# Optimization experiments

Measured on AMD Instinct MI355X. Metric: run time of the kernel, lower is better.

## Reference

```python
import jax, jax.numpy as jnp
import numpy as np

N, D = 8192, 256

def _gram_rbf(x, y, sigma):
    x2 = jnp.sum(x * x, axis=-1)                      # [N]
    y2 = jnp.sum(y * y, axis=-1)                      # [M]
    xy = jnp.einsum('nd,md->nm', x, y)                # [N,M] GEMM
    sq = x2[:, None] + y2[None, :] - 2.0 * xy
    return jnp.exp(-sq / sigma)

def setup_inputs() -> dict:
    key = jax.random.key(0)
    k1, k2 = jax.random.split(key)
    return {
        'input': jax.random.normal(k1, (N, D), dtype=jnp.float32),
        'target': jax.random.normal(k2, (N, D), dtype=jnp.float32) + 0.5,
        'sigma': 256,
    }

def reference(input, target, sigma):
    XX = _gram_rbf(input, input, sigma)
    YY = _gram_rbf(target, target, sigma)
    XY = _gram_rbf(input, target, sigma)
    return jnp.mean(XX) + jnp.mean(YY) - 2.0 * jnp.mean(XY)
```

## Files before the change

kernel.cpp:

```cpp
#include <hip/hip_runtime.h>
#include <hip/hip_bf16.h>
#include <stdint.h>
#include <stddef.h>


#define N_PTS   8192
#define DIM     256
#define TWO_N   16384
#define CSTRIDE 20

#define AS1 __attribute__((address_space(1)))
#define AS3 __attribute__((address_space(3)))

typedef __attribute__((ext_vector_type(4))) float f32x4;
typedef __attribute__((ext_vector_type(4))) int   i32x4;
typedef __attribute__((ext_vector_type(8))) int   i32x8;

__global__ __launch_bounds__(256) void mmd_prep(const float* __restrict__ X,
                                                const float* __restrict__ Y,
                                                const int* __restrict__ sigmap,
                                                unsigned char* __restrict__ Zf8,
                                                float* __restrict__ n2,
                                                float* __restrict__ part) {
    if (blockIdx.x == 0 && threadIdx.x < 64) part[threadIdx.x] = 0.0f;

    const int wave = threadIdx.x >> 6;
    const int lane = threadIdx.x & 63;
    const int row  = blockIdx.x * 4 + wave;

    const float* src = (row < N_PTS) ? (X + (size_t)row * DIM)
                                     : (Y + (size_t)(row - N_PTS) * DIM);
    float4 v = ((const float4*)src)[lane];

    float s = v.x * v.x + v.y * v.y + v.z * v.z + v.w * v.w;
#pragma unroll
    for (int off = 32; off; off >>= 1) s += __shfl_down(s, off, 64);
    if (lane == 0) {
        const float c2 = -1.4426950408889634f / (float)(*sigmap);
        n2[row] = c2 * s;
    }

    const int p01 = __builtin_amdgcn_cvt_pk_fp8_f32(v.x, v.y, 0, false);
    const int p23 = __builtin_amdgcn_cvt_pk_fp8_f32(v.z, v.w, 0, false);
    const unsigned int pk = ((unsigned)p01 & 0xffffu) | ((unsigned)p23 << 16);
    *(unsigned int*)(Zf8 + (size_t)row * DIM + (size_t)lane * 4) = pk;
}

__global__ __launch_bounds__(256, 5) void mmd_main(const unsigned char* __restrict__ Zf8,
                                                   const float* __restrict__ n2,
                                                   const int* __restrict__ sigmap,
                                                   float* __restrict__ part) {
    __shared__ char smem_b[32768];

    const int bid = (int)blockIdx.x;
    const int p   = bid / CSTRIDE;
    const int cc  = bid % CSTRIDE;
    const int r0  = p;
    const int r1  = 127 - p;

    const int nT0 = (cc <= r0) ? ((r0 - cc) / CSTRIDE + 1) : 0;
    const int nT1 = (r1 - cc) / CSTRIDE + 1;
    const int nS0 = nT0 * 2;
    const int nS  = nS0 + nT1 * 2;

    const int t    = threadIdx.x;
    const int wave = t >> 6;
    const int lane = t & 63;
    const int g    = lane >> 4;
    const int ml   = lane & 15;

    const float m2 = 2.8853900817779268f / (float)(*sigmap);
    const int   SC = 0x7f7f7f7f;

    const int gbase = (t >> 4) * 256 + (((t & 15) ^ (t >> 4)) * 16);
    const int lbase = t * 16;

    int rb0[2], rb1[2];
#pragma unroll
    for (int kc = 0; kc < 2; ++kc) {
        rb0[kc] = ml * 256 + (((kc * 8 + g * 2)     ^ ml) * 16);
        rb1[kc] = ml * 256 + (((kc * 8 + g * 2 + 1) ^ ml) * 16);
    }

    i32x8 af[2][2];
    float a_i[2][4];
    auto loadA = [&](int rowTile) {
        const int rowBase = rowTile * 128;
#pragma unroll
        for (int mt = 0; mt < 2; ++mt) {
            const unsigned char* rp =
                Zf8 + (size_t)(rowBase + wave * 32 + mt * 16 + ml) * 256 + g * 32;
#pragma unroll
            for (int kc = 0; kc < 2; ++kc) {
                union { i32x4 h[2]; i32x8 v; } u;
                u.h[0] = *(const i32x4*)(rp + kc * 128);
                u.h[1] = *(const i32x4*)(rp + kc * 128 + 16);
                af[mt][kc] = u.v;
            }
        }
#pragma unroll
        for (int mt = 0; mt < 2; ++mt)
#pragma unroll
            for (int rr = 0; rr < 4; ++rr)
                a_i[mt][rr] = n2[rowBase + wave * 32 + mt * 16 + g * 4 + rr];
    };

    const int firstRow = nT0 ? r0 : r1;
    loadA(firstRow);
    int curRow = firstRow;

    const f32x4 zacc = {0.0f, 0.0f, 0.0f, 0.0f};

    auto sliceCol = [&](int s, int& rowT, int& bc, int& h) {
        int si;
        if (s < nS0) { rowT = r0; si = s; }
        else         { rowT = r1; si = s - nS0; }
        bc = cc + (si >> 1) * CSTRIDE;
        h  = si & 1;
    };

    {
        int rT, bc, h; sliceCol(0, rT, bc, h);
        const unsigned char* sb = Zf8 + (size_t)(bc * 128 + h * 64) * 256 + gbase;
#pragma unroll
        for (int i = 0; i < 4; ++i)
            __builtin_amdgcn_global_load_lds((const AS1 void*)(sb + i * 4096),
                                             (AS3 void*)(smem_b + i * 4096 + lbase), 16, 0, 0);
    }

    float block_acc = 0.0f;
    int cur = 0;

    for (int s = 0; s < nS; ++s) {
        int rowT, bc, h;
        sliceCol(s, rowT, bc, h);
        if (rowT != curRow) { loadA(rowT); curRow = rowT; }
        const int colBase = bc * 128 + h * 64;

        float eb[4];
#pragma unroll
        for (int nt = 0; nt < 4; ++nt)
            eb[nt] = __builtin_amdgcn_exp2f(n2[colBase + nt * 16 + ml]);

        __syncthreads();

        if (s + 1 < nS) {
            int rTN, bcN, hN;
            sliceCol(s + 1, rTN, bcN, hN);
            const unsigned char* sb =
                Zf8 + (size_t)(bcN * 128 + hN * 64) * 256 + gbase;
            char* dst = smem_b + (cur ^ 1) * 16384;
#pragma unroll
            for (int i = 0; i < 4; ++i)
                __builtin_amdgcn_global_load_lds((const AS1 void*)(sb + i * 4096),
                                                 (AS3 void*)(dst + i * 4096 + lbase), 16, 0, 0);
        }

        const char* buf = smem_b + cur * 16384;
        f32x4 acc[2][4];
#pragma unroll
        for (int nt = 0; nt < 4; ++nt) {
#pragma unroll
            for (int kc = 0; kc < 2; ++kc) {
                union { i32x4 hh[2]; i32x8 v; } u;
                u.hh[0] = *(const i32x4*)(buf + nt * 4096 + rb0[kc]);
                u.hh[1] = *(const i32x4*)(buf + nt * 4096 + rb1[kc]);
                const i32x8 bf = u.v;
#pragma unroll
                for (int mt = 0; mt < 2; ++mt)
                    acc[mt][nt] = __builtin_amdgcn_mfma_scale_f32_16x16x128_f8f6f4(
                        af[mt][kc], bf, (kc == 0) ? zacc : acc[mt][nt],
                        0, 0, 0, SC, 0, SC);
            }
        }

        float ts0 = 0.0f, ts1 = 0.0f, ts2 = 0.0f, ts3 = 0.0f;
#pragma unroll
        for (int mt = 0; mt < 2; ++mt)
#pragma unroll
            for (int nt = 0; nt < 4; ++nt) {
                const float e = eb[nt];
                ts0 = fmaf(__builtin_amdgcn_exp2f(fmaf(acc[mt][nt][0], m2, a_i[mt][0])), e, ts0);
                ts1 = fmaf(__builtin_amdgcn_exp2f(fmaf(acc[mt][nt][1], m2, a_i[mt][1])), e, ts1);
                ts2 = fmaf(__builtin_amdgcn_exp2f(fmaf(acc[mt][nt][2], m2, a_i[mt][2])), e, ts2);
                ts3 = fmaf(__builtin_amdgcn_exp2f(fmaf(acc[mt][nt][3], m2, a_i[mt][3])), e, ts3);
            }
        const float tsum = (ts0 + ts1) + (ts2 + ts3);

        const float sgn = ((bc < 64) == (rowT < 64)) ? 1.0f : -1.0f;
        const float w   = (bc == rowT) ? sgn : 2.0f * sgn;
        block_acc = fmaf(w, tsum, block_acc);
        cur ^= 1;
    }

    float s = block_acc;
#pragma unroll
    for (int off = 32; off; off >>= 1) s += __shfl_down(s, off, 64);
    if (lane == 0)
        atomicAdd(part + (bid & 63), s);
}

__global__ __launch_bounds__(64) void mmd_finish(const float* __restrict__ part,
                                                 float* __restrict__ out) {
    const int lane = threadIdx.x & 63;
    float s = part[lane];
#pragma unroll
    for (int off = 32; off; off >>= 1) s += __shfl_down(s, off, 64);
    if (lane == 0) out[0] = s * (1.0f / 67108864.0f);
}

extern "C" void kernel_launch(void* const* d_in, const int* in_sizes, int n_in,
                              void* d_out, int out_size, void* d_ws, size_t ws_size,
                              hipStream_t stream) {
    const float* X      = (const float*)d_in[0];
    const float* Y      = (const float*)d_in[1];
    const int*   sigmap = (const int*)d_in[2];
    float*       out    = (float*)d_out;

    unsigned char* Zf8  = (unsigned char*)d_ws;
    float*         n2   = (float*)((char*)d_ws + (size_t)TWO_N * DIM);
    float*         part = n2 + TWO_N;

    mmd_prep<<<TWO_N / 4, 256, 0, stream>>>(X, Y, sigmap, Zf8, n2, part);
    mmd_main<<<64 * CSTRIDE, 256, 0, stream>>>(Zf8, n2, sigmap, part);
    mmd_finish<<<1, 64, 0, stream>>>(part, out);
}
```

Baseline: 136.5 us.

## Load B tiles directly from global into registers and split work across 2048 blocks

Drops the double-buffered LDS staging of the B operand via global_load_lds and its per-slice barrier. Each wave now reads its B fragments straight from global memory (through L2/L1) into registers. The grid changes from 20 column strides to 16, and each block's slice list is split in two halves, giving 2048 blocks with occupancy hint 4. This removes the barrier and LDS traffic. The cost is that B is no longer shared across the four waves, so global and L1 loads are duplicated and load latency is exposed without explicit prefetch.

```diff
diff --git a/kernel.cpp b/kernel.cpp
--- a/kernel.cpp
+++ b/kernel.cpp
@@ -7,10 +7,6 @@
 #define N_PTS   8192
 #define DIM     256
 #define TWO_N   16384
-#define CSTRIDE 20
-
-#define AS1 __attribute__((address_space(1)))
-#define AS3 __attribute__((address_space(3)))
 
 typedef __attribute__((ext_vector_type(4))) float f32x4;
 typedef __attribute__((ext_vector_type(4))) int   i32x4;
@@ -46,22 +42,23 @@
     *(unsigned int*)(Zf8 + (size_t)row * DIM + (size_t)lane * 4) = pk;
 }
 
-__global__ __launch_bounds__(256, 5) void mmd_main(const unsigned char* __restrict__ Zf8,
+__global__ __launch_bounds__(256, 4) void mmd_main(const unsigned char* __restrict__ Zf8,
                                                    const float* __restrict__ n2,
                                                    const int* __restrict__ sigmap,
                                                    float* __restrict__ part) {
-    __shared__ char smem_b[32768];
-
     const int bid = (int)blockIdx.x;
-    const int p   = bid / CSTRIDE;
-    const int cc  = bid % CSTRIDE;
+    const int p   = bid >> 5;
+    const int cc  = (bid >> 1) & 15;
+    const int hb  = bid & 1;
     const int r0  = p;
     const int r1  = 127 - p;
 
-    const int nT0 = (cc <= r0) ? ((r0 - cc) / CSTRIDE + 1) : 0;
-    const int nT1 = (r1 - cc) / CSTRIDE + 1;
+    const int nT0 = (cc <= r0) ? (((r0 - cc) >> 4) + 1) : 0;
+    const int nT1 = ((r1 - cc) >> 4) + 1;
     const int nS0 = nT0 * 2;
     const int nS  = nS0 + nT1 * 2;
+    const int sBeg = hb ? (nS >> 1) : 0;
+    const int sEnd = hb ? nS : (nS >> 1);
 
     const int t    = threadIdx.x;
     const int wave = t >> 6;
@@ -71,16 +68,6 @@
 
     const float m2 = 2.8853900817779268f / (float)(*sigmap);
     const int   SC = 0x7f7f7f7f;
-
-    const int gbase = (t >> 4) * 256 + (((t & 15) ^ (t >> 4)) * 16);
-    const int lbase = t * 16;
-
-    int rb0[2], rb1[2];
-#pragma unroll
-    for (int kc = 0; kc < 2; ++kc) {
-        rb0[kc] = ml * 256 + (((kc * 8 + g * 2)     ^ ml) * 16);
-        rb1[kc] = ml * 256 + (((kc * 8 + g * 2 + 1) ^ ml) * 16);
-    }
 
     i32x8 af[2][2];
     float a_i[2][4];
@@ -105,33 +92,25 @@
                 a_i[mt][rr] = n2[rowBase + wave * 32 + mt * 16 + g * 4 + rr];
     };
 
-    const int firstRow = nT0 ? r0 : r1;
-    loadA(firstRow);
-    int curRow = firstRow;
-
-    const f32x4 zacc = {0.0f, 0.0f, 0.0f, 0.0f};
-
     auto sliceCol = [&](int s, int& rowT, int& bc, int& h) {
         int si;
         if (s < nS0) { rowT = r0; si = s; }
         else         { rowT = r1; si = s - nS0; }
-        bc = cc + (si >> 1) * CSTRIDE;
+        bc = cc + (si >> 1) * 16;
         h  = si & 1;
     };
 
-    {
-        int rT, bc, h; sliceCol(0, rT, bc, h);
-        const unsigned char* sb = Zf8 + (size_t)(bc * 128 + h * 64) * 256 + gbase;
-#pragma unroll
-        for (int i = 0; i < 4; ++i)
-            __builtin_amdgcn_global_load_lds((const AS1 void*)(sb + i * 4096),
-                                             (AS3 void*)(smem_b + i * 4096 + lbase), 16, 0, 0);
-    }
+    int rT0, bc0, h0;
+    sliceCol(sBeg, rT0, bc0, h0);
+    loadA(rT0);
+    int curRow = rT0;
+
+    const f32x4 zacc = {0.0f, 0.0f, 0.0f, 0.0f};
+    const int laneB = ml * 256 + g * 32;
 
     float block_acc = 0.0f;
-    int cur = 0;
 
-    for (int s = 0; s < nS; ++s) {
+    for (int s = sBeg; s < sEnd; ++s) {
         int rowT, bc, h;
         sliceCol(s, rowT, bc, h);
         if (rowT != curRow) { loadA(rowT); curRow = rowT; }
@@ -142,29 +121,16 @@
         for (int nt = 0; nt < 4; ++nt)
             eb[nt] = __builtin_amdgcn_exp2f(n2[colBase + nt * 16 + ml]);
 
-        __syncthreads();
+        const unsigned char* sp = Zf8 + (size_t)colBase * 256 + laneB;
 
-        if (s + 1 < nS) {
-            int rTN, bcN, hN;
-            sliceCol(s + 1, rTN, bcN, hN);
-            const unsigned char* sb =
-                Zf8 + (size_t)(bcN * 128 + hN * 64) * 256 + gbase;
-            char* dst = smem_b + (cur ^ 1) * 16384;
-#pragma unroll
-            for (int i = 0; i < 4; ++i)
-                __builtin_amdgcn_global_load_lds((const AS1 void*)(sb + i * 4096),
-                                                 (AS3 void*)(dst + i * 4096 + lbase), 16, 0, 0);
-        }
-
-        const char* buf = smem_b + cur * 16384;
         f32x4 acc[2][4];
 #pragma unroll
         for (int nt = 0; nt < 4; ++nt) {
 #pragma unroll
             for (int kc = 0; kc < 2; ++kc) {
                 union { i32x4 hh[2]; i32x8 v; } u;
-                u.hh[0] = *(const i32x4*)(buf + nt * 4096 + rb0[kc]);
-                u.hh[1] = *(const i32x4*)(buf + nt * 4096 + rb1[kc]);
+                u.hh[0] = *(const i32x4*)(sp + nt * 4096 + kc * 128);
+                u.hh[1] = *(const i32x4*)(sp + nt * 4096 + kc * 128 + 16);
                 const i32x8 bf = u.v;
 #pragma unroll
                 for (int mt = 0; mt < 2; ++mt)
@@ -190,7 +156,6 @@
         const float sgn = ((bc < 64) == (rowT < 64)) ? 1.0f : -1.0f;
         const float w   = (bc == rowT) ? sgn : 2.0f * sgn;
         block_acc = fmaf(w, tsum, block_acc);
-        cur ^= 1;
     }
 
     float s = block_acc;
@@ -222,6 +187,6 @@
     float*         part = n2 + TWO_N;
 
     mmd_prep<<<TWO_N / 4, 256, 0, stream>>>(X, Y, sigmap, Zf8, n2, part);
-    mmd_main<<<64 * CSTRIDE, 256, 0, stream>>>(Zf8, n2, sigmap, part);
+    mmd_main<<<64 * 16 * 2, 256, 0, stream>>>(Zf8, n2, sigmap, part);
     mmd_finish<<<1, 64, 0, stream>>>(part, out);
 }
```

After: 213.9 us. 1.57x slower.
